# Performance work log

Measured on AMD Instinct MI355X. Metric: run time of the kernel, lower is better.

The kernel has to match this reference:

```python
import jax, jax.numpy as jnp
import numpy as np

N = 100000      # total nodes
E = 800000      # directed edges
DIN = 256       # input feature dim
H = 128         # hidden dim
EPS = 1e-5      # BatchNorm eps


def setup_inputs() -> dict:
    key = jax.random.key(0)
    ks = jax.random.split(key, 18)
    s = 0.05
    return {
        "x": jax.random.normal(ks[0], (N, DIN), jnp.float32),
        "src": jax.random.randint(ks[1], (E,), 0, N, dtype=jnp.int32),
        "dst": jax.random.randint(ks[2], (E,), 0, N, dtype=jnp.int32),
        "W1": jax.random.normal(ks[3], (DIN, H), jnp.float32) * s,
        "b1": jnp.zeros((H,), jnp.float32),
        "g1": jnp.ones((H,), jnp.float32),
        "be1": jnp.zeros((H,), jnp.float32),
        "W2": jax.random.normal(ks[4], (H, H), jnp.float32) * s,
        "b2": jnp.zeros((H,), jnp.float32),
        "g2": jnp.ones((H,), jnp.float32),
        "be2": jnp.zeros((H,), jnp.float32),
        "W3": jax.random.normal(ks[5], (H, H), jnp.float32) * s,
        "b3": jnp.zeros((H,), jnp.float32),
        "g3": jnp.ones((H,), jnp.float32),
        "be3": jnp.zeros((H,), jnp.float32),
        "Wf": jax.random.normal(ks[6], (H, 1), jnp.float32) * s,
        "bf": jnp.zeros((1,), jnp.float32),
    }


def _gcn_conv(h, W, b, src, dst, dis):
    # GCNConv: project, then sym-normalized aggregation over edges + self-loops
    h = h @ W                                   # [N, out]
    coef = dis[src] * dis[dst]                  # [E] edge norm weights
    agg = jax.ops.segment_sum(h[src] * coef[:, None], dst, num_segments=N)
    agg = agg + h * (dis * dis)[:, None]        # self-loop term (norm = 1/deg)
    return agg + b


def _bn_relu(h, g, be):
    # BatchNorm1d in training mode (batch stats over nodes, biased variance)
    mu = jnp.mean(h, axis=0)
    var = jnp.var(h, axis=0)
    return jax.nn.relu((h - mu) * (g / jnp.sqrt(var + EPS)) + be)


def reference(x, src, dst, W1, b1, g1, be1, W2, b2, g2, be2,
              W3, b3, g3, be3, Wf, bf):
    # degree of (A + I) counted on destination nodes, edge weight 1
    deg = jax.ops.segment_sum(jnp.ones((E,), jnp.float32), dst, num_segments=N) + 1.0
    dis = jax.lax.rsqrt(deg)                    # deg >= 1, safe

    h = _bn_relu(_gcn_conv(x, W1, b1, src, dst, dis), g1, be1)
    h = _bn_relu(_gcn_conv(h, W2, b2, src, dst, dis), g2, be2)
    h = _bn_relu(_gcn_conv(h, W3, b3, src, dst, dis), g3, be3)
    return h @ Wf + bf                          # [N, 1]
```

## Files before the change

### kernel.cpp

```cpp
#include <hip/hip_runtime.h>
#include <hip/hip_bf16.h>

typedef unsigned short ushort_t;
typedef __bf16 bf16x8 __attribute__((ext_vector_type(8)));
typedef unsigned short ushort8 __attribute__((ext_vector_type(8)));
typedef unsigned short ushort4v __attribute__((ext_vector_type(4)));
typedef float f32x4 __attribute__((ext_vector_type(4)));

#define HH 128
#define EPS 1e-5f
#define STAT_SLICES 32

__device__ __forceinline__ float bf2f(ushort_t u) {
    unsigned v = ((unsigned)u) << 16;
    return __builtin_bit_cast(float, v);
}
__device__ __forceinline__ ushort_t f2bf(float f) {
    unsigned u = __builtin_bit_cast(unsigned, f);
    unsigned r = (u + 0x7fffu + ((u >> 16) & 1u)) >> 16;
    return (ushort_t)r;
}
__device__ __forceinline__ float cvt(const void* p, int i, int flag) {
    return flag ? bf2f(((const ushort_t*)p)[i]) : ((const float*)p)[i];
}

__global__ void preK(const int* __restrict__ dst, int* __restrict__ counts, int E,
                     const void* W1, ushort_t* Wt1, const void* W2, ushort_t* Wt2,
                     const void* W3, ushort_t* Wt3,
                     const void* g1, const void* b1, const void* b2, const void* b3,
                     const void* g2, const void* g3, const void* be1, const void* be2,
                     const void* be3, const void* Wfp, const void* bfp,
                     float* __restrict__ cvec, int histB) {
    const int bid = blockIdx.x;
    const int tid = threadIdx.x;
    const int flag = (((const ushort_t*)g1)[0] == 0x3F80) ? 1 : 0;
    if (bid < histB) {
        int e = bid * 256 + tid;
        if (e < E) atomicAdd(&counts[dst[e]], 1);
    } else if (bid < histB + 256) {
        int idx = (bid - histB) * 256 + tid;
        const void* W; ushort_t* Wt; int Kp;
        if (idx < 32768)      { W = W1; Wt = Wt1; Kp = 264; }
        else if (idx < 49152) { W = W2; Wt = Wt2; Kp = 136; idx -= 32768; }
        else                  { W = W3; Wt = Wt3; Kp = 136; idx -= 49152; }
        int k = idx >> 7, nn = idx & 127;
        Wt[nn * Kp + k] = flag ? ((const ushort_t*)W)[idx] : f2bf(((const float*)W)[idx]);
    } else {
        int t = tid;
        if (t < 128) {
            cvec[t]        = cvt(b1, t, flag);
            cvec[128 + t]  = cvt(b2, t, flag);
            cvec[256 + t]  = cvt(b3, t, flag);
            cvec[384 + t]  = cvt(g1, t, flag);
            cvec[512 + t]  = cvt(g2, t, flag);
            cvec[640 + t]  = cvt(g3, t, flag);
            cvec[768 + t]  = cvt(be1, t, flag);
            cvec[896 + t]  = cvt(be2, t, flag);
            cvec[1024 + t] = cvt(be3, t, flag);
            cvec[1152 + t] = cvt(Wfp, t, flag);
            if (t == 0) cvec[1280] = cvt(bfp, 0, flag);
        }
    }
}

__global__ void scanAdisK(const int* __restrict__ cnt, int* __restrict__ partial,
                          float* __restrict__ dis, int n, int nbScan) {
    __shared__ int lds[256];
    const int tid = threadIdx.x;
    if ((int)blockIdx.x < nbScan) {
        int base = blockIdx.x * 2048 + tid * 8;
        int s = 0;
#pragma unroll
        for (int j = 0; j < 8; ++j) { int idx = base + j; if (idx < n) s += cnt[idx]; }
        lds[tid] = s; __syncthreads();
        for (int off = 128; off; off >>= 1) { if (tid < off) lds[tid] += lds[tid + off]; __syncthreads(); }
        if (tid == 0) partial[blockIdx.x] = lds[0];
    } else {
        int i = (blockIdx.x - nbScan) * 256 + tid;
        if (i < n) dis[i] = rsqrtf((float)cnt[i] + 1.0f);
    }
}

__global__ void scanB(int* __restrict__ partial, int* __restrict__ rowptr, int nb, int n) {
    if (threadIdx.x == 0) {
        int running = 0;
        for (int i = 0; i < nb; ++i) { int v = partial[i]; partial[i] = running; running += v; }
        rowptr[n] = running;
    }
}

__device__ __forceinline__ void scanCDev(int* lds, const int* __restrict__ cnt,
                                         const int* __restrict__ partial,
                                         int* __restrict__ rowptr, int n, int bid) {
    const int tid = threadIdx.x;
    int base = bid * 2048 + tid * 8;
    int v[8]; int s = 0;
#pragma unroll
    for (int j = 0; j < 8; ++j) { int idx = base + j; v[j] = (idx < n) ? cnt[idx] : 0; s += v[j]; }
    lds[tid] = s; __syncthreads();
    for (int off = 1; off < 256; off <<= 1) {
        int x = (tid >= off) ? lds[tid - off] : 0;
        __syncthreads();
        lds[tid] += x;
        __syncthreads();
    }
    int excl = lds[tid] - s;
    int off0 = partial[bid] + excl;
#pragma unroll
    for (int j = 0; j < 8; ++j) {
        int idx = base + j;
        if (idx < n) { rowptr[idx] = off0; off0 += v[j]; }
    }
}

__global__ void scatterK(const int* __restrict__ src, const int* __restrict__ dst,
                         const int* __restrict__ rowptr, int* __restrict__ fill,
                         const float* __restrict__ dis,
                         uint2* __restrict__ erec, int E) {
    int e = blockIdx.x * 256 + threadIdx.x;
    if (e >= E) return;
    int d = dst[e], s = src[e];
    int old = atomicSub(&fill[d], 1);
    int pos = rowptr[d] + old - 1;
    float c = dis[s] * dis[d];
    uint2 r; r.x = (unsigned)s; r.y = __builtin_bit_cast(unsigned, c);
    erec[pos] = r;
}

template <bool BN, bool EXT, int K>
__device__ __forceinline__ void mmDev(char* smemRaw, const void* __restrict__ Av,
                                      const ushort_t* __restrict__ Wt,
                                      ushort_t* __restrict__ out, int n,
                                      const float* __restrict__ ssum,
                                      const float* __restrict__ ssq,
                                      const float* __restrict__ gam,
                                      const float* __restrict__ bet,
                                      const ushort_t* __restrict__ flagRef, int bid) {
    constexpr int KP  = K + 8;
    constexpr int BKP = 136;
    constexpr int NCH = K / 128;
    constexpr int NST = K / 32;

    ushort_t* bs = (ushort_t*)smemRaw;
    float* scw = (float*)(smemRaw + 128 * BKP * 2);

    const int tid  = threadIdx.x;
    const int lane = tid & 63;
    const int wave = tid >> 6;
    const int m = lane & 15;
    const int q = lane >> 4;

    if constexpr (BN) {
        if (tid < 128) {
            float S = 0.f, Q = 0.f;
#pragma unroll
            for (int sl = 0; sl < STAT_SLICES; ++sl) { S += ssum[sl * HH + tid]; Q += ssq[sl * HH + tid]; }
            float invn = 1.0f / (float)n;
            float mu = S * invn;
            float var = fmaxf(Q * invn - mu * mu, 0.f);
            float sc = gam[tid] * rsqrtf(var + EPS);
            scw[tid] = sc;
            scw[128 + tid] = bet[tid] - mu * sc;
        }
        __syncthreads();
    }

    const int flag = EXT ? ((flagRef[0] == 0x3F80) ? 1 : 0) : 1;

    int rowA = bid * 64 + wave * 16 + m;
    int rA = rowA < n ? rowA : (n - 1);

    ushort8 a[NST];
    if (EXT && !flag) {
        const float* ap32 = (const float*)Av + (size_t)rA * K + q * 8;
#pragma unroll
        for (int s = 0; s < NST; ++s) {
            float4 f0 = *(const float4*)(ap32 + s * 32);
            float4 f1 = *(const float4*)(ap32 + s * 32 + 4);
            a[s][0] = f2bf(f0.x); a[s][1] = f2bf(f0.y); a[s][2] = f2bf(f0.z); a[s][3] = f2bf(f0.w);
            a[s][4] = f2bf(f1.x); a[s][5] = f2bf(f1.y); a[s][6] = f2bf(f1.z); a[s][7] = f2bf(f1.w);
        }
    } else {
        const ushort_t* ap16 = (const ushort_t*)Av + (size_t)rA * K + q * 8;
#pragma unroll
        for (int s = 0; s < NST; ++s) a[s] = *(const ushort8*)(ap16 + s * 32);
    }
    if constexpr (BN) {
#pragma unroll
        for (int s = 0; s < NST; ++s) {
            int kb = s * 32 + q * 8;
#pragma unroll
            for (int j = 0; j < 8; ++j) {
                float f = fmaxf(bf2f(a[s][j]) * scw[kb + j] + scw[128 + kb + j], 0.f);
                a[s][j] = f2bf(f);
            }
        }
    }

    f32x4 acc[8];
#pragma unroll
    for (int t = 0; t < 8; ++t) acc[t] = (f32x4){0.f, 0.f, 0.f, 0.f};

#pragma unroll
    for (int c = 0; c < NCH; ++c) {
#pragma unroll
        for (int r = 0; r < 8; ++r) {
            int idx = tid + r * 256;
            int row = idx >> 4, seg = idx & 15;
            *(uint4*)&bs[row * BKP + seg * 8] =
                *(const uint4*)&Wt[(size_t)row * KP + c * 128 + seg * 8];
        }
        __syncthreads();
#pragma unroll
        for (int s = 0; s < 4; ++s) {
            bf16x8 nf = __builtin_bit_cast(bf16x8, a[c * 4 + s]);
#pragma unroll
            for (int t = 0; t < 8; ++t) {
                ushort8 wv = *(const ushort8*)&bs[(t * 16 + m) * BKP + s * 32 + q * 8];
                acc[t] = __builtin_amdgcn_mfma_f32_16x16x32_bf16(
                    __builtin_bit_cast(bf16x8, wv), nf, acc[t], 0, 0, 0);
            }
        }
        if (c + 1 < NCH) __syncthreads();
    }

    const int node_g = bid * 64 + wave * 16 + m;
    if (node_g < n) {
        ushort_t* op = out + (size_t)node_g * HH + q * 4;
#pragma unroll
        for (int t = 0; t < 8; ++t) {
            ushort4v pk;
#pragma unroll
            for (int r = 0; r < 4; ++r) pk[r] = f2bf(acc[t][r]);
            *(ushort4v*)(op + t * 16) = pk;
        }
    }
}

__global__ __launch_bounds__(256) void mm1scanCK(const void* __restrict__ x,
                                                 const ushort_t* __restrict__ Wt1,
                                                 ushort_t* __restrict__ tbuf, int n,
                                                 const ushort_t* __restrict__ flagRef,
                                                 const int* __restrict__ cnt,
                                                 const int* __restrict__ partial,
                                                 int* __restrict__ rowptr, int mmB) {
    __shared__ char smem[35840];
    if ((int)blockIdx.x < mmB)
        mmDev<false, true, 256>(smem, x, Wt1, tbuf, n, nullptr, nullptr, nullptr, nullptr,
                                flagRef, blockIdx.x);
    else
        scanCDev((int*)smem, cnt, partial, rowptr, n, blockIdx.x - mmB);
}

template <int K>
__global__ __launch_bounds__(256) void mmBNK(const ushort_t* __restrict__ A,
                                             const ushort_t* __restrict__ Wt,
                                             ushort_t* __restrict__ out, int n,
                                             const float* __restrict__ ssum,
                                             const float* __restrict__ ssq,
                                             const float* __restrict__ gam,
                                             const float* __restrict__ bet) {
    __shared__ char smem[35840];
    mmDev<true, false, K>(smem, A, Wt, out, n, ssum, ssq, gam, bet, nullptr, blockIdx.x);
}

__global__ __launch_bounds__(256) void aggK(const ushort_t* __restrict__ t,
                                            const uint2* __restrict__ erec,
                                            const int* __restrict__ rowptr,
                                            const float* __restrict__ dis,
                                            const float* __restrict__ bias,
                                            ushort_t* __restrict__ g,
                                            float* __restrict__ ssum, float* __restrict__ ssq,
                                            int n) {
    const int lane = threadIdx.x & 63;
    const int wave = threadIdx.x >> 6;
    const int cb = lane * 2;
    const float b0 = bias[cb], b1 = bias[cb + 1];
    float s0 = 0.f, s1 = 0.f, q0 = 0.f, q1 = 0.f;

    for (int node = blockIdx.x * 4 + wave; node < n; node += gridDim.x * 4) {
        float d = dis[node];
        float d2 = d * d;
        unsigned sv = *(const unsigned*)(t + (size_t)node * HH + cb);
        float a0 = bf2f((ushort_t)(sv & 0xffff)) * d2;
        float a1 = bf2f((ushort_t)(sv >> 16)) * d2;

        int beg = rowptr[node], end = rowptr[node + 1];
        for (int eb = beg; eb < end; eb += 64) {
            int rem = end - eb; if (rem > 64) rem = 64;
            uint2 rec = (lane < rem) ? erec[eb + lane] : (uint2){0u, 0u};
            int es = (int)rec.x;
            float ec = __builtin_bit_cast(float, rec.y);
            int rr = (rem + 7) & ~7;
            for (int j = 0; j < rr; j += 8) {
                int ii[8]; float cc[8]; unsigned ww[8];
#pragma unroll
                for (int k = 0; k < 8; ++k) {
                    ii[k] = __shfl(es, j + k);
                    cc[k] = __shfl(ec, j + k);
                }
#pragma unroll
                for (int k = 0; k < 8; ++k)
                    ww[k] = *(const unsigned*)(t + (size_t)ii[k] * HH + cb);
#pragma unroll
                for (int k = 0; k < 8; ++k) {
                    a0 += bf2f((ushort_t)(ww[k] & 0xffff)) * cc[k];
                    a1 += bf2f((ushort_t)(ww[k] >> 16)) * cc[k];
                }
            }
        }
        a0 += b0; a1 += b1;
        unsigned packed = (unsigned)f2bf(a0) | ((unsigned)f2bf(a1) << 16);
        *(unsigned*)(g + (size_t)node * HH + cb) = packed;
        s0 += a0; s1 += a1; q0 += a0 * a0; q1 += a1 * a1;
    }

    __shared__ float red[4][64][4];
    red[wave][lane][0] = s0; red[wave][lane][1] = s1;
    red[wave][lane][2] = q0; red[wave][lane][3] = q1;
    __syncthreads();
    if (wave == 0) {
        float S0 = 0, S1 = 0, Q0 = 0, Q1 = 0;
#pragma unroll
        for (int w = 0; w < 4; ++w) {
            S0 += red[w][lane][0]; S1 += red[w][lane][1];
            Q0 += red[w][lane][2]; Q1 += red[w][lane][3];
        }
        int slice = (blockIdx.x & (STAT_SLICES - 1)) * HH;
        atomicAdd(&ssum[slice + cb], S0);
        atomicAdd(&ssum[slice + cb + 1], S1);
        atomicAdd(&ssq[slice + cb], Q0);
        atomicAdd(&ssq[slice + cb + 1], Q1);
    }
}

__global__ __launch_bounds__(256) void outK(const ushort_t* __restrict__ g,
                                            const float* __restrict__ ssum,
                                            const float* __restrict__ ssq,
                                            const float* __restrict__ gam,
                                            const float* __restrict__ bet,
                                            const float* __restrict__ Wf,
                                            const float* __restrict__ bfp,
                                            void* __restrict__ outv, int n,
                                            const ushort_t* __restrict__ flagRef) {
    __shared__ float scw[256];
    const int tid = threadIdx.x;
    if (tid < 128) {
        float S = 0.f, Q = 0.f;
#pragma unroll
        for (int sl = 0; sl < STAT_SLICES; ++sl) { S += ssum[sl * HH + tid]; Q += ssq[sl * HH + tid]; }
        float invn = 1.0f / (float)n;
        float mu = S * invn;
        float var = fmaxf(Q * invn - mu * mu, 0.f);
        float sc = gam[tid] * rsqrtf(var + EPS);
        scw[tid] = sc;
        scw[128 + tid] = bet[tid] - mu * sc;
    }
    __syncthreads();

    const int lane = tid & 63;
    const int wave = tid >> 6;
    const int cb = lane * 2;
    const float w0 = Wf[cb], w1 = Wf[cb + 1];
    const float sc0 = scw[cb], sc1 = scw[cb + 1];
    const float sh0 = scw[128 + cb], sh1 = scw[128 + cb + 1];
    const float bb = bfp[0];
    const int flag = (flagRef[0] == 0x3F80) ? 1 : 0;

    for (int node = blockIdx.x * 4 + wave; node < n; node += gridDim.x * 4) {
        unsigned v = *(const unsigned*)(g + (size_t)node * HH + cb);
        float h0 = fmaxf(bf2f((ushort_t)(v & 0xffff)) * sc0 + sh0, 0.f);
        float h1 = fmaxf(bf2f((ushort_t)(v >> 16)) * sc1 + sh1, 0.f);
        float x = h0 * w0 + h1 * w1;
#pragma unroll
        for (int off = 32; off; off >>= 1) x += __shfl_down(x, off);
        if (lane == 0) {
            float r = x + bb;
            if (flag) ((ushort_t*)outv)[node] = f2bf(r);
            else      ((float*)outv)[node] = r;
        }
    }
}

extern "C" void kernel_launch(void* const* d_in, const int* in_sizes, int n_in,
                              void* d_out, int out_size, void* d_ws, size_t ws_size,
                              hipStream_t stream) {
    const int DIN = 256;
    const int N = in_sizes[0] / DIN;
    const int E = in_sizes[1];

    const void* x   = d_in[0];
    const int*  src = (const int*)d_in[1];
    const int*  dst = (const int*)d_in[2];
    const void* W1  = d_in[3];
    const void* b1  = d_in[4];
    const void* g1  = d_in[5];
    const void* be1 = d_in[6];
    const void* W2  = d_in[7];
    const void* b2  = d_in[8];
    const void* g2  = d_in[9];
    const void* be2 = d_in[10];
    const void* W3  = d_in[11];
    const void* b3  = d_in[12];
    const void* g3  = d_in[13];
    const void* be3 = d_in[14];
    const void* Wf  = d_in[15];
    const void* bfp = d_in[16];
    const ushort_t* flagRef = (const ushort_t*)g1;

    char* base = (char*)d_ws;
    size_t off = 0;
    auto carve = [&](size_t bytes) -> void* {
        void* p = base + off;
        off += (bytes + 255) & ~(size_t)255;
        return p;
    };
    int*      counts = (int*)carve((size_t)N * 4);
    float*    stats  = (float*)carve((size_t)3 * 2 * STAT_SLICES * HH * 4);
    size_t    zbytes = off;
    float*    dis    = (float*)carve((size_t)N * 4);
    int*      rowptr = (int*)carve((size_t)(N + 1) * 4);
    int*      partial= (int*)carve(256 * 4);
    uint2*    erec   = (uint2*)carve((size_t)E * 8);
    ushort_t* Wt1    = (ushort_t*)carve((size_t)128 * 264 * 2);
    ushort_t* Wt2    = (ushort_t*)carve((size_t)128 * 136 * 2);
    ushort_t* Wt3    = (ushort_t*)carve((size_t)128 * 136 * 2);
    ushort_t* tbuf   = (ushort_t*)carve((size_t)N * HH * 2);
    ushort_t* gbuf   = (ushort_t*)carve((size_t)N * HH * 2);
    float*    cvec   = (float*)carve((size_t)1281 * 4);

    float* ssum0 = stats;                         float* ssq0 = ssum0 + STAT_SLICES * HH;
    float* ssum1 = ssq0 + STAT_SLICES * HH;       float* ssq1 = ssum1 + STAT_SLICES * HH;
    float* ssum2 = ssq1 + STAT_SLICES * HH;       float* ssq2 = ssum2 + STAT_SLICES * HH;

    float* c_b1 = cvec;         float* c_b2 = cvec + 128;  float* c_b3 = cvec + 256;
    float* c_g1 = cvec + 384;   float* c_g2 = cvec + 512;  float* c_g3 = cvec + 640;
    float* c_be1 = cvec + 768;  float* c_be2 = cvec + 896; float* c_be3 = cvec + 1024;
    float* c_Wf = cvec + 1152;  float* c_bf = cvec + 1280;

    const int nbScan = (N + 2047) / 2048;
    const int histB  = (E + 255) / 256;
    const int disB   = (N + 255) / 256;
    const int mmB    = (N + 63) / 64;
    const int aggB   = 2048;

    hipMemsetAsync(d_ws, 0, zbytes, stream);

    preK<<<histB + 256 + 1, 256, 0, stream>>>(dst, counts, E, W1, Wt1, W2, Wt2, W3, Wt3,
                                              g1, b1, b2, b3, g2, g3, be1, be2, be3, Wf, bfp,
                                              cvec, histB);
    scanAdisK<<<nbScan + disB, 256, 0, stream>>>(counts, partial, dis, N, nbScan);
    scanB<<<1, 64, 0, stream>>>(partial, rowptr, nbScan, N);
    mm1scanCK<<<mmB + nbScan, 256, 0, stream>>>(x, Wt1, tbuf, N, flagRef,
                                                counts, partial, rowptr, mmB);
    scatterK<<<histB, 256, 0, stream>>>(src, dst, rowptr, counts, dis, erec, E);

    aggK<<<aggB, 256, 0, stream>>>(tbuf, erec, rowptr, dis, c_b1, gbuf, ssum0, ssq0, N);
    mmBNK<128><<<mmB, 256, 0, stream>>>(gbuf, Wt2, tbuf, N, ssum0, ssq0, c_g1, c_be1);
    aggK<<<aggB, 256, 0, stream>>>(tbuf, erec, rowptr, dis, c_b2, gbuf, ssum1, ssq1, N);
    mmBNK<128><<<mmB, 256, 0, stream>>>(gbuf, Wt3, tbuf, N, ssum1, ssq1, c_g2, c_be2);
    aggK<<<aggB, 256, 0, stream>>>(tbuf, erec, rowptr, dis, c_b3, gbuf, ssum2, ssq2, N);
    outK<<<1024, 256, 0, stream>>>(gbuf, ssum2, ssq2, c_g3, c_be3, c_Wf, c_bf, d_out, N, flagRef);
}
```

Measured before the change: 459.5 us.

## Double rows per GEMM wave, widen aggregation gathers, fold scanB into scanC

The GEMM kernels now compute two 16-row fragments per wave (128 rows per block), so each B-tile read from LDS feeds two MFMAs and the grid halves. The aggregation kernel has each half-wave handle alternate edges with 8-byte (4-channel) gathers and combines the halves with a cross-lane shuffle, which changes the per-lane load width and memory-level parallelism. The serial scanB launch is removed, and each scan block recomputes its prefix from the partial sums. The trade-offs are higher register pressure in the GEMM and redundant prefix loops in the scan blocks.

```diff
diff --git a/kernel.cpp b/kernel.cpp
--- a/kernel.cpp
+++ b/kernel.cpp
@@ -81,18 +81,12 @@
     }
 }
 
-__global__ void scanB(int* __restrict__ partial, int* __restrict__ rowptr, int nb, int n) {
-    if (threadIdx.x == 0) {
-        int running = 0;
-        for (int i = 0; i < nb; ++i) { int v = partial[i]; partial[i] = running; running += v; }
-        rowptr[n] = running;
-    }
-}
-
-__device__ __forceinline__ void scanCDev(int* lds, const int* __restrict__ cnt,
-                                         const int* __restrict__ partial,
-                                         int* __restrict__ rowptr, int n, int bid) {
+__device__ __forceinline__ void scanC2Dev(int* lds, const int* __restrict__ cnt,
+                                          const int* __restrict__ partial,
+                                          int* __restrict__ rowptr, int n, int bid, int nb) {
     const int tid = threadIdx.x;
+    int pre = 0, tot = 0;
+    for (int i = 0; i < nb; ++i) { int v = partial[i]; if (i < bid) pre += v; tot += v; }
     int base = bid * 2048 + tid * 8;
     int v[8]; int s = 0;
 #pragma unroll
@@ -105,12 +99,13 @@
         __syncthreads();
     }
     int excl = lds[tid] - s;
-    int off0 = partial[bid] + excl;
+    int off0 = pre + excl;
 #pragma unroll
     for (int j = 0; j < 8; ++j) {
         int idx = base + j;
         if (idx < n) { rowptr[idx] = off0; off0 += v[j]; }
     }
+    if (bid == 0 && tid == 0) rowptr[n] = tot;
 }
 
 __global__ void scatterK(const int* __restrict__ src, const int* __restrict__ dst,
@@ -167,23 +162,30 @@
 
     const int flag = EXT ? ((flagRef[0] == 0x3F80) ? 1 : 0) : 1;
 
-    int rowA = bid * 64 + wave * 16 + m;
-    int rA = rowA < n ? rowA : (n - 1);
-
-    ushort8 a[NST];
+    const int base = bid * 128 + wave * 32 + m;
+    int r0 = base < n ? base : (n - 1);
+    int r1 = (base + 16) < n ? (base + 16) : (n - 1);
+
+    ushort8 a0[NST], a1[NST];
     if (EXT && !flag) {
-        const float* ap32 = (const float*)Av + (size_t)rA * K + q * 8;
+        const float* p0 = (const float*)Av + (size_t)r0 * K + q * 8;
+        const float* p1 = (const float*)Av + (size_t)r1 * K + q * 8;
 #pragma unroll
         for (int s = 0; s < NST; ++s) {
-            float4 f0 = *(const float4*)(ap32 + s * 32);
-            float4 f1 = *(const float4*)(ap32 + s * 32 + 4);
-            a[s][0] = f2bf(f0.x); a[s][1] = f2bf(f0.y); a[s][2] = f2bf(f0.z); a[s][3] = f2bf(f0.w);
-            a[s][4] = f2bf(f1.x); a[s][5] = f2bf(f1.y); a[s][6] = f2bf(f1.z); a[s][7] = f2bf(f1.w);
+            float4 f0 = *(const float4*)(p0 + s * 32);
+            float4 f1 = *(const float4*)(p0 + s * 32 + 4);
+            float4 g0 = *(const float4*)(p1 + s * 32);
+            float4 g1v = *(const float4*)(p1 + s * 32 + 4);
+            a0[s][0] = f2bf(f0.x); a0[s][1] = f2bf(f0.y); a0[s][2] = f2bf(f0.z); a0[s][3] = f2bf(f0.w);
+            a0[s][4] = f2bf(f1.x); a0[s][5] = f2bf(f1.y); a0[s][6] = f2bf(f1.z); a0[s][7] = f2bf(f1.w);
+            a1[s][0] = f2bf(g0.x); a1[s][1] = f2bf(g0.y); a1[s][2] = f2bf(g0.z); a1[s][3] = f2bf(g0.w);
+            a1[s][4] = f2bf(g1v.x); a1[s][5] = f2bf(g1v.y); a1[s][6] = f2bf(g1v.z); a1[s][7] = f2bf(g1v.w);
         }
     } else {
-        const ushort_t* ap16 = (const ushort_t*)Av + (size_t)rA * K + q * 8;
-#pragma unroll
-        for (int s = 0; s < NST; ++s) a[s] = *(const ushort8*)(ap16 + s * 32);
+        const ushort_t* p0 = (const ushort_t*)Av + (size_t)r0 * K + q * 8;
+        const ushort_t* p1 = (const ushort_t*)Av + (size_t)r1 * K + q * 8;
+#pragma unroll
+        for (int s = 0; s < NST; ++s) { a0[s] = *(const ushort8*)(p0 + s * 32); a1[s] = *(const ushort8*)(p1 + s * 32); }
     }
     if constexpr (BN) {
 #pragma unroll
@@ -191,15 +193,16 @@
             int kb = s * 32 + q * 8;
 #pragma unroll
             for (int j = 0; j < 8; ++j) {
-                float f = fmaxf(bf2f(a[s][j]) * scw[kb + j] + scw[128 + kb + j], 0.f);
-                a[s][j] = f2bf(f);
+                float sc = scw[kb + j], sh = scw[128 + kb + j];
+                a0[s][j] = f2bf(fmaxf(bf2f(a0[s][j]) * sc + sh, 0.f));
+                a1[s][j] = f2bf(fmaxf(bf2f(a1[s][j]) * sc + sh, 0.f));
             }
         }
     }
 
-    f32x4 acc[8];
-#pragma unroll
-    for (int t = 0; t < 8; ++t) acc[t] = (f32x4){0.f, 0.f, 0.f, 0.f};
+    f32x4 acc0[8], acc1[8];
+#pragma unroll
+    for (int t = 0; t < 8; ++t) { acc0[t] = (f32x4){0.f,0.f,0.f,0.f}; acc1[t] = (f32x4){0.f,0.f,0.f,0.f}; }
 
 #pragma unroll
     for (int c = 0; c < NCH; ++c) {
@@ -213,26 +216,31 @@
         __syncthreads();
 #pragma unroll
         for (int s = 0; s < 4; ++s) {
-            bf16x8 nf = __builtin_bit_cast(bf16x8, a[c * 4 + s]);
+            bf16x8 nf0 = __builtin_bit_cast(bf16x8, a0[c * 4 + s]);
+            bf16x8 nf1 = __builtin_bit_cast(bf16x8, a1[c * 4 + s]);
 #pragma unroll
             for (int t = 0; t < 8; ++t) {
                 ushort8 wv = *(const ushort8*)&bs[(t * 16 + m) * BKP + s * 32 + q * 8];
-                acc[t] = __builtin_amdgcn_mfma_f32_16x16x32_bf16(
-                    __builtin_bit_cast(bf16x8, wv), nf, acc[t], 0, 0, 0);
+                bf16x8 wb = __builtin_bit_cast(bf16x8, wv);
+                acc0[t] = __builtin_amdgcn_mfma_f32_16x16x32_bf16(wb, nf0, acc0[t], 0, 0, 0);
+                acc1[t] = __builtin_amdgcn_mfma_f32_16x16x32_bf16(wb, nf1, acc1[t], 0, 0, 0);
             }
         }
         if (c + 1 < NCH) __syncthreads();
     }
 
-    const int node_g = bid * 64 + wave * 16 + m;
-    if (node_g < n) {
-        ushort_t* op = out + (size_t)node_g * HH + q * 4;
-#pragma unroll
-        for (int t = 0; t < 8; ++t) {
-            ushort4v pk;
-#pragma unroll
-            for (int r = 0; r < 4; ++r) pk[r] = f2bf(acc[t][r]);
-            *(ushort4v*)(op + t * 16) = pk;
+#pragma unroll
+    for (int f = 0; f < 2; ++f) {
+        int node_g = base + f * 16;
+        if (node_g < n) {
+            ushort_t* op = out + (size_t)node_g * HH + q * 4;
+#pragma unroll
+            for (int t = 0; t < 8; ++t) {
+                ushort4v pk;
+#pragma unroll
+                for (int r = 0; r < 4; ++r) pk[r] = f2bf(f == 0 ? acc0[t][r] : acc1[t][r]);
+                *(ushort4v*)(op + t * 16) = pk;
+            }
         }
     }
 }
@@ -243,13 +251,13 @@
                                                  const ushort_t* __restrict__ flagRef,
                                                  const int* __restrict__ cnt,
                                                  const int* __restrict__ partial,
-                                                 int* __restrict__ rowptr, int mmB) {
+                                                 int* __restrict__ rowptr, int mmB, int nbScan) {
     __shared__ char smem[35840];
     if ((int)blockIdx.x < mmB)
         mmDev<false, true, 256>(smem, x, Wt1, tbuf, n, nullptr, nullptr, nullptr, nullptr,
                                 flagRef, blockIdx.x);
     else
-        scanCDev((int*)smem, cnt, partial, rowptr, n, blockIdx.x - mmB);
+        scanC2Dev((int*)smem, cnt, partial, rowptr, n, blockIdx.x - mmB, nbScan);
 }
 
 template <int K>
@@ -274,16 +282,18 @@
                                             int n) {
     const int lane = threadIdx.x & 63;
     const int wave = threadIdx.x >> 6;
-    const int cb = lane * 2;
-    const float b0 = bias[cb], b1 = bias[cb + 1];
-    float s0 = 0.f, s1 = 0.f, q0 = 0.f, q1 = 0.f;
+    const int h = lane >> 5;
+    const int c4 = (lane & 31) * 4;
+    float bv[4];
+#pragma unroll
+    for (int i = 0; i < 4; ++i) bv[i] = bias[c4 + i];
+    float st[4] = {0.f,0.f,0.f,0.f}, sq[4] = {0.f,0.f,0.f,0.f};
 
     for (int node = blockIdx.x * 4 + wave; node < n; node += gridDim.x * 4) {
         float d = dis[node];
         float d2 = d * d;
-        unsigned sv = *(const unsigned*)(t + (size_t)node * HH + cb);
-        float a0 = bf2f((ushort_t)(sv & 0xffff)) * d2;
-        float a1 = bf2f((ushort_t)(sv >> 16)) * d2;
+        uint2 sv = *(const uint2*)(t + (size_t)node * HH + c4);
+        float a[4] = {0.f,0.f,0.f,0.f};
 
         int beg = rowptr[node], end = rowptr[node + 1];
         for (int eb = beg; eb < end; eb += 64) {
@@ -291,46 +301,58 @@
             uint2 rec = (lane < rem) ? erec[eb + lane] : (uint2){0u, 0u};
             int es = (int)rec.x;
             float ec = __builtin_bit_cast(float, rec.y);
-            int rr = (rem + 7) & ~7;
-            for (int j = 0; j < rr; j += 8) {
-                int ii[8]; float cc[8]; unsigned ww[8];
+            int rr = (rem + 15) & ~15;
+            for (int j = 0; j < rr; j += 16) {
+                int ii[8]; float cf[8]; uint2 w[8];
 #pragma unroll
                 for (int k = 0; k < 8; ++k) {
-                    ii[k] = __shfl(es, j + k);
-                    cc[k] = __shfl(ec, j + k);
+                    int e = j + 2 * k + h;
+                    ii[k] = __shfl(es, e);
+                    cf[k] = __shfl(ec, e);
                 }
 #pragma unroll
                 for (int k = 0; k < 8; ++k)
-                    ww[k] = *(const unsigned*)(t + (size_t)ii[k] * HH + cb);
+                    w[k] = *(const uint2*)(t + (size_t)ii[k] * HH + c4);
 #pragma unroll
                 for (int k = 0; k < 8; ++k) {
-                    a0 += bf2f((ushort_t)(ww[k] & 0xffff)) * cc[k];
-                    a1 += bf2f((ushort_t)(ww[k] >> 16)) * cc[k];
+                    a[0] += bf2f((ushort_t)(w[k].x & 0xffff)) * cf[k];
+                    a[1] += bf2f((ushort_t)(w[k].x >> 16)) * cf[k];
+                    a[2] += bf2f((ushort_t)(w[k].y & 0xffff)) * cf[k];
+                    a[3] += bf2f((ushort_t)(w[k].y >> 16)) * cf[k];
                 }
             }
         }
-        a0 += b0; a1 += b1;
-        unsigned packed = (unsigned)f2bf(a0) | ((unsigned)f2bf(a1) << 16);
-        *(unsigned*)(g + (size_t)node * HH + cb) = packed;
-        s0 += a0; s1 += a1; q0 += a0 * a0; q1 += a1 * a1;
-    }
-
-    __shared__ float red[4][64][4];
-    red[wave][lane][0] = s0; red[wave][lane][1] = s1;
-    red[wave][lane][2] = q0; red[wave][lane][3] = q1;
+#pragma unroll
+        for (int i = 0; i < 4; ++i) a[i] += __shfl(a[i], lane ^ 32);
+        a[0] += bf2f((ushort_t)(sv.x & 0xffff)) * d2 + bv[0];
+        a[1] += bf2f((ushort_t)(sv.x >> 16)) * d2 + bv[1];
+        a[2] += bf2f((ushort_t)(sv.y & 0xffff)) * d2 + bv[2];
+        a[3] += bf2f((ushort_t)(sv.y >> 16)) * d2 + bv[3];
+        if (h == 0) {
+            uint2 pk;
+            pk.x = (unsigned)f2bf(a[0]) | ((unsigned)f2bf(a[1]) << 16);
+            pk.y = (unsigned)f2bf(a[2]) | ((unsigned)f2bf(a[3]) << 16);
+            *(uint2*)(g + (size_t)node * HH + c4) = pk;
+#pragma unroll
+            for (int i = 0; i < 4; ++i) { st[i] += a[i]; sq[i] += a[i] * a[i]; }
+        }
+    }
+
+    __shared__ float red[4][32][8];
+    if (h == 0) {
+#pragma unroll
+        for (int i = 0; i < 4; ++i) { red[wave][lane & 31][i] = st[i]; red[wave][lane & 31][4 + i] = sq[i]; }
+    }
     __syncthreads();
-    if (wave == 0) {
-        float S0 = 0, S1 = 0, Q0 = 0, Q1 = 0;
-#pragma unroll
-        for (int w = 0; w < 4; ++w) {
-            S0 += red[w][lane][0]; S1 += red[w][lane][1];
-            Q0 += red[w][lane][2]; Q1 += red[w][lane][3];
-        }
+    if (threadIdx.x < 128) {
+        int ch = threadIdx.x;
+        int l = ch >> 2, i = ch & 3;
+        float S = 0.f, Q = 0.f;
+#pragma unroll
+        for (int w = 0; w < 4; ++w) { S += red[w][l][i]; Q += red[w][l][4 + i]; }
         int slice = (blockIdx.x & (STAT_SLICES - 1)) * HH;
-        atomicAdd(&ssum[slice + cb], S0);
-        atomicAdd(&ssum[slice + cb + 1], S1);
-        atomicAdd(&ssq[slice + cb], Q0);
-        atomicAdd(&ssq[slice + cb + 1], Q1);
+        atomicAdd(&ssum[slice + ch], S);
+        atomicAdd(&ssq[slice + ch], Q);
     }
 }
 
@@ -441,7 +463,7 @@
     const int nbScan = (N + 2047) / 2048;
     const int histB  = (E + 255) / 256;
     const int disB   = (N + 255) / 256;
-    const int mmB    = (N + 63) / 64;
+    const int mmB    = (N + 127) / 128;
     const int aggB   = 2048;
 
     hipMemsetAsync(d_ws, 0, zbytes, stream);
@@ -450,9 +472,8 @@
                                               g1, b1, b2, b3, g2, g3, be1, be2, be3, Wf, bfp,
                                               cvec, histB);
     scanAdisK<<<nbScan + disB, 256, 0, stream>>>(counts, partial, dis, N, nbScan);
-    scanB<<<1, 64, 0, stream>>>(partial, rowptr, nbScan, N);
     mm1scanCK<<<mmB + nbScan, 256, 0, stream>>>(x, Wt1, tbuf, N, flagRef,
-                                                counts, partial, rowptr, mmB);
+                                                counts, partial, rowptr, mmB, nbScan);
     scatterK<<<histB, 256, 0, stream>>>(src, dst, rowptr, counts, dis, erec, E);
 
     aggK<<<aggB, 256, 0, stream>>>(tbuf, erec, rowptr, dis, c_b1, gbuf, ssum0, ssq0, N);
```

Measured after the change: 496.7 us. 8.1% more time.
